# Optimization experiments

Measured on AMD Instinct MI355X. Metric: run time of the kernel, lower is better.

The kernel has to match this reference:

```python
import jax, jax.numpy as jnp
import numpy as np

B, S, D_MODEL, N_HEADS = 4, 2048, 512, 2
D4 = D_MODEL * 4            # output dim of quaternion projections (2048)
HD = D4 // N_HEADS          # per-head dim (1024)
EPS = 1e-6


def quat_linear(x, W, b):
    """Hamilton-product quaternion linear.
    x: [..., 4*in_q] (quaternions interleaved r,i,j,k)
    W: [4, out_q, in_q] components (r,i,j,k); b: [4*out_q]
    returns [..., 4*out_q]
    """
    xq = x.reshape(x.shape[:-1] + (-1, 4))
    xr, xi, xj, xk = xq[..., 0], xq[..., 1], xq[..., 2], xq[..., 3]
    Wr, Wi, Wj, Wk = W[0], W[1], W[2], W[3]
    m = lambda a, M: jnp.einsum('...i,oi->...o', a, M)
    o_r = m(xr, Wr) - m(xi, Wi) - m(xj, Wj) - m(xk, Wk)
    o_i = m(xr, Wi) + m(xi, Wr) + m(xj, Wk) - m(xk, Wj)
    o_j = m(xr, Wj) - m(xi, Wk) + m(xj, Wr) + m(xk, Wi)
    o_k = m(xr, Wk) + m(xi, Wj) - m(xj, Wi) + m(xk, Wr)
    out = jnp.stack([o_r, o_i, o_j, o_k], axis=-1)
    return out.reshape(out.shape[:-2] + (-1,)) + b


def setup_inputs() -> dict:
    rng = jax.random.key(0)
    ks = jax.random.split(rng, 12)
    def w(k, out_q, in_q):
        return jax.random.normal(k, (4, out_q, in_q), jnp.float32) * (1.0 / np.sqrt(4.0 * in_q))
    in_q_small = D_MODEL // 4   # q/k/v projections: d_model reals -> d_model quaternions
    in_q_big = D4 // 4          # later projections: 4*d_model reals -> d_model quaternions
    zb = jnp.zeros((D4,), jnp.float32)
    return {
        'query': jax.random.normal(ks[0], (B, S, D_MODEL), jnp.float32),
        'key':   jax.random.normal(ks[1], (B, S, D_MODEL), jnp.float32),
        'value': jax.random.normal(ks[2], (B, S, D_MODEL), jnp.float32),
        'Wq': w(ks[3], D_MODEL, in_q_small), 'bq': zb,
        'Wk': w(ks[4], D_MODEL, in_q_small), 'bk': zb,
        'Wv': w(ks[5], D_MODEL, in_q_small), 'bv': zb,
        'alpha': jax.random.normal(ks[6], (D4,), jnp.float32) * 0.1,
        'Wint': w(ks[7], D_MODEL, in_q_big), 'bint': zb,
        'Wfin': w(ks[8], D_MODEL, in_q_big), 'bfin': zb,
        'Wout': w(ks[9], D_MODEL, in_q_big), 'bout': zb,
    }


def reference(query, key, value, Wq, bq, Wk, bk, Wv, bv, alpha,
              Wint, bint, Wfin, bfin, Wout, bout):
    Q = quat_linear(query, Wq, bq).reshape(B, S, N_HEADS, HD)
    K = quat_linear(key, Wk, bk).reshape(B, S, N_HEADS, HD)
    V = quat_linear(value, Wv, bv).reshape(B, S, N_HEADS, HD)

    # spectral attention: FFT correlation + adaptive spectral filter
    Qf = jnp.fft.fft(Q, axis=1)
    Kf = jnp.fft.fft(K, axis=1)
    corr = Qf * jnp.conj(Kf)                        # [B,S,H,HD] complex64
    freqs = jnp.abs(jnp.fft.fftfreq(S))             # [S]
    phase = jnp.arctan(jnp.log(freqs + EPS))        # [S]
    a = alpha.reshape(N_HEADS, HD)
    filt = jnp.exp(1j * (phase[:, None, None] * a[None, :, :]))  # [S,H,HD]
    attn_w = jnp.fft.ifft(corr * filt[None], axis=1).real        # [B,S,H,HD]
    attn = (attn_w * V).reshape(B, S, -1)           # [B,S,4*d_model]

    attn = quat_linear(attn, Wint, bint)
    attn = quat_linear(attn, Wfin, bfin)
    return quat_linear(attn, Wout, bout)            # [B,S,4*d_model]
```

## Files before the change

### kernel.cpp

```cpp
#include <hip/hip_runtime.h>
#include <hip/hip_bf16.h>
#include <cstdint>

typedef unsigned short u16;
typedef u16  u16x8 __attribute__((ext_vector_type(8)));
typedef short s16x8 __attribute__((ext_vector_type(8)));
typedef float f32x4 __attribute__((ext_vector_type(4)));

#define PI_F 3.14159265358979323846f
#define PD(i) ((i) + 3 * ((i) >> 5))

static __device__ __forceinline__ u16 f2bf(float f) {
    union { float f; unsigned u; } v; v.f = f;
    unsigned r = v.u + 0x7fffu + ((v.u >> 16) & 1u);
    return (u16)(r >> 16);
}
static __device__ __forceinline__ float bf2f(u16 h) {
    union { unsigned u; float f; } v; v.u = ((unsigned)h) << 16;
    return v.f;
}

__device__ __forceinline__ void gl_lds16(const u16* g, u16* l) {
    __builtin_amdgcn_global_load_lds(
        (const __attribute__((address_space(1))) unsigned int*)g,
        (__attribute__((address_space(3))) unsigned int*)l, 16, 0, 0);
}

__device__ __forceinline__ void cvt_body(int blk, const float* __restrict__ in,
                                         u16* __restrict__ o) {
    int i = blk * 256 + threadIdx.x;
    float4 a = ((const float4*)in)[2 * i];
    float4 b = ((const float4*)in)[2 * i + 1];
    u16x8 vv;
    vv[0] = f2bf(a.x); vv[1] = f2bf(a.y); vv[2] = f2bf(a.z); vv[3] = f2bf(a.w);
    vv[4] = f2bf(b.x); vv[5] = f2bf(b.y); vv[6] = f2bf(b.z); vv[7] = f2bf(b.w);
    ((u16x8*)o)[i] = vv;
}

template<int LOGK>
__device__ __forceinline__ void e3_body(int blk, const float* __restrict__ W,
                                        u16* __restrict__ E) {
    const int K = 1 << LOGK;
    int idx = blk * 256 + threadIdx.x;
    int n = idx >> LOGK, k = idx & (K - 1);
    int o = n >> 2, c = n & 3, i = k >> 2, cp = k & 3;
    const int   qm[4][4] = {{0,1,2,3},{1,0,3,2},{2,3,0,1},{3,2,1,0}};
    const float qs[4][4] = {{1.f,-1.f,-1.f,-1.f},{1.f,1.f,1.f,-1.f},
                            {1.f,-1.f,1.f,1.f},{1.f,1.f,-1.f,1.f}};
    int in_q = K >> 2;
    float w = W[(size_t)qm[c][cp] * 512 * in_q + (size_t)o * in_q + i] * qs[c][cp];
    E[idx] = f2bf(w);
}

__device__ __forceinline__ void tabs_body(int blk, float2* __restrict__ gws,
                                          float* __restrict__ ph) {
    int i = blk * 256 + threadIdx.x;
    if (i < 682) {
        int off, lh;
        if (i < 2)        { off = 0;   lh = 1; }
        else if (i < 10)  { off = 2;   lh = 3; }
        else if (i < 42)  { off = 10;  lh = 5; }
        else if (i < 170) { off = 42;  lh = 7; }
        else              { off = 170; lh = 9; }
        int j = i - off;
        float a = (-PI_F) * (float)j / (float)(2 << lh);
        gws[i] = make_float2(cosf(a), sinf(a));
    }
    if (i <= 1024) {
        ph[i] = atanf(logf((float)i * (1.0f / 2048.0f) + 1e-6f));
    }
}

__global__ __launch_bounds__(256) void fat_prep(
        const float* __restrict__ query, const float* __restrict__ key,
        const float* __restrict__ value, u16* __restrict__ Acvt,
        const float* __restrict__ Wq, const float* __restrict__ Wk,
        const float* __restrict__ Wv, u16* __restrict__ Eq,
        u16* __restrict__ Ek, u16* __restrict__ Ev,
        const float* __restrict__ Wint, const float* __restrict__ Wfin,
        const float* __restrict__ Wout, u16* __restrict__ Eint,
        u16* __restrict__ Efin, u16* __restrict__ Eout,
        float2* __restrict__ gws, float* __restrict__ pht) {
    int b = blockIdx.x;
    if (b < 6144) {
        int ten = b >> 11, r = b & 2047;
        const float* in = (ten == 0) ? query : (ten == 1) ? key : value;
        cvt_body(r, in, Acvt + (size_t)ten * 8192 * 512);
    } else if (b < 18432) {
        int rb = b - 6144;
        int y = rb >> 12, r = rb & 4095;
        e3_body<9>(r, (y == 0) ? Wq : (y == 1) ? Wk : Wv,
                   (y == 0) ? Eq : (y == 1) ? Ek : Ev);
    } else if (b < 67584) {
        int rb = b - 18432;
        int y = rb >> 14, r = rb & 16383;
        e3_body<11>(r, (y == 0) ? Wint : (y == 1) ? Wfin : Wout,
                    (y == 0) ? Eint : (y == 1) ? Efin : Eout);
    } else {
        tabs_body(b - 67584, gws, pht);
    }
}

__global__ __launch_bounds__(256) void matvec_E(const float* __restrict__ v,
                                                const u16* __restrict__ E,
                                                const float* __restrict__ badd,
                                                float* __restrict__ out) {
    int n    = (blockIdx.x * 256 + threadIdx.x) >> 6;
    int lane = threadIdx.x & 63;
    if (n >= 2048) return;
    const u16* row = E + (size_t)n * 2048;
    float s = 0.f;
    for (int j = lane; j < 2048; j += 64) s += v[j] * bf2f(row[j]);
#pragma unroll
    for (int o = 32; o; o >>= 1) s += __shfl_down(s, o, 64);
    if (lane == 0) out[n] = s + badd[n];
}

template<int K, int OUTMODE, int NBY>
__device__ __forceinline__ void gemm_body(int bid, u16* As, u16* Bs,
                                          const u16* __restrict__ A,
                                          const u16* __restrict__ E,
                                          const float* __restrict__ bias,
                                          void* __restrict__ outp) {
    const int t    = threadIdx.x;
    const int lane = t & 63, wave = t >> 6;
    const int wr   = wave >> 1, wc = wave & 1;
    const int lr   = lane & 15, kg = lane >> 4;
    const int l7   = lr & 7;

    constexpr int SPX = (4 * (NBY / 4)) / 8;
    const int xcd = bid & 7, p = bid >> 3;
    const int st  = xcd * SPX + (p >> 4);
    const int w   = p & 15;
    const int bx  = (st & 3) * 4 + (w & 3);
    const int by  = (st >> 2) * 4 + (w >> 2);
    const int m0  = by * 128;
    const int n0  = bx * 128;

    f32x4 acc[4][4];
#pragma unroll
    for (int i = 0; i < 4; ++i)
#pragma unroll
        for (int j = 0; j < 4; ++j) acc[i][j] = (f32x4){0.f, 0.f, 0.f, 0.f};

    const int arow = wr * 64 + lr;
    const int brow = wc * 64 + lr;

    for (int k0 = 0; k0 < K; k0 += 64) {
#pragma unroll
        for (int c = 0; c < 4; ++c) {
            int idx = t + c * 256;
            int row = idx >> 3, sl = idx & 7;
            int gsl = sl ^ (row & 7);
            gl_lds16(A + (size_t)(m0 + row) * K + k0 + gsl * 8, &As[idx * 8]);
            gl_lds16(E + (size_t)(n0 + row) * K + k0 + gsl * 8, &Bs[idx * 8]);
        }
        __syncthreads();
#pragma unroll
        for (int ks = 0; ks < 2; ++ks) {
            const int slot = (ks * 4 + kg) ^ l7;
            s16x8 av[4], bv[4];
#pragma unroll
            for (int mi = 0; mi < 4; ++mi)
                av[mi] = *(const s16x8*)&As[(arow + mi * 16) * 64 + slot * 8];
#pragma unroll
            for (int ni = 0; ni < 4; ++ni)
                bv[ni] = *(const s16x8*)&Bs[(brow + ni * 16) * 64 + slot * 8];
#pragma unroll
            for (int mi = 0; mi < 4; ++mi)
#pragma unroll
                for (int ni = 0; ni < 4; ++ni)
                    acc[mi][ni] = __builtin_amdgcn_mfma_f32_16x16x32_bf16(
                        av[mi], bv[ni], acc[mi][ni], 0, 0, 0);
        }
        __syncthreads();
    }

#pragma unroll
    for (int ni = 0; ni < 4; ++ni) {
        int n = n0 + wc * 64 + ni * 16 + lr;
        float bvl = bias ? bias[n] : 0.0f;
#pragma unroll
        for (int mi = 0; mi < 4; ++mi) {
#pragma unroll
            for (int r = 0; r < 4; ++r) {
                int m = m0 + wr * 64 + mi * 16 + kg * 4 + r;
                float val = acc[mi][ni][r] + bvl;
                if constexpr (OUTMODE == 0) {
                    ((u16*)outp)[(size_t)m * 2048 + n] = f2bf(val);
                } else if constexpr (OUTMODE == 1) {
                    ((float*)outp)[(size_t)m * 2048 + n] = val;
                } else {
                    int b = m >> 11, s = m & 2047;
                    ((u16*)outp)[((size_t)b * 2048 + n) * 2048 + s] = f2bf(val);
                }
            }
        }
    }
}

template<int K, int OUTMODE, int NBY>
__global__ __launch_bounds__(256) void gemm2(const u16* __restrict__ A,
                                             const u16* __restrict__ E,
                                             const float* __restrict__ bias,
                                             void* __restrict__ outp) {
    __shared__ u16 As[128 * 64];
    __shared__ u16 Bs[128 * 64];
    gemm_body<K, OUTMODE, NBY>(blockIdx.x, As, Bs, A, E, bias, outp);
}

__global__ __launch_bounds__(256) void gemm_fat1(const u16* __restrict__ Aq,
                                                 const u16* __restrict__ Eq,
                                                 const float* __restrict__ bq,
                                                 void* __restrict__ Qt,
                                                 const u16* __restrict__ Efin,
                                                 const u16* __restrict__ EintT,
                                                 void* __restrict__ T1T) {
    __shared__ u16 As[128 * 64];
    __shared__ u16 Bs[128 * 64];
    int bid = blockIdx.x;
    if (bid < 256)
        gemm_body<2048, 2, 16>(bid, As, Bs, Efin, EintT, nullptr, T1T);
    else
        gemm_body<512, 2, 64>(bid - 256, As, Bs, Aq, Eq, bq, Qt);
}

__global__ __launch_bounds__(256) void gemm_fat2(const u16* __restrict__ Ak,
                                                 const u16* __restrict__ Ek,
                                                 const float* __restrict__ bk,
                                                 void* __restrict__ Kt,
                                                 const u16* __restrict__ Eout,
                                                 const u16* __restrict__ T1T,
                                                 void* __restrict__ Ecomb) {
    __shared__ u16 As[128 * 64];
    __shared__ u16 Bs[128 * 64];
    int bid = blockIdx.x;
    if (bid < 256)
        gemm_body<2048, 0, 16>(bid, As, Bs, Eout, T1T, nullptr, Ecomb);
    else
        gemm_body<512, 2, 64>(bid - 256, As, Bs, Ak, Ek, bk, Kt);
}

template<int LH, int OFF>
__device__ __forceinline__ void r4pass(float* re, float* im,
                                       const float2* __restrict__ wt, int t) {
    constexpr int h = 1 << LH;
    __syncthreads();
#pragma unroll
    for (int u = 0; u < 2; ++u) {
        int vidx = t + u * 256;
        int j = vidx & (h - 1);
        int i0 = ((vidx >> LH) << (LH + 2)) | j;
        float2 w2 = wt[OFF + j];
        float w1r = w2.x * w2.x - w2.y * w2.y;
        float w1i = 2.f * w2.x * w2.y;
        float w3r = w2.y, w3i = -w2.x;
        int p0 = PD(i0), p1 = PD(i0 + h), p2 = PD(i0 + 2 * h), p3 = PD(i0 + 3 * h);
        float ar = re[p0], ai = im[p0];
        float br = re[p1], bi = im[p1];
        float cr = re[p2], ci = im[p2];
        float dr = re[p3], di = im[p3];
        float tbr = w1r * br - w1i * bi, tbi = w1r * bi + w1i * br;
        float tdr = w1r * dr - w1i * di, tdi = w1r * di + w1i * dr;
        float a1r = ar + tbr, a1i = ai + tbi;
        float b1r = ar - tbr, b1i = ai - tbi;
        float c1r = cr + tdr, c1i = ci + tdi;
        float d1r = cr - tdr, d1i = ci - tdi;
        float tcr = w2.x * c1r - w2.y * c1i, tci = w2.x * c1i + w2.y * c1r;
        float ter = w3r * d1r - w3i * d1i, tei = w3r * d1i + w3i * d1r;
        re[p0] = a1r + tcr; im[p0] = a1i + tci;
        re[p2] = a1r - tcr; im[p2] = a1i - tci;
        re[p1] = b1r + ter; im[p1] = b1i + tei;
        re[p3] = b1r - ter; im[p3] = b1i - tei;
    }
}

__device__ void fft2048(float* re, float* im, const float2* __restrict__ wt, int t) {
    __syncthreads();
#pragma unroll
    for (int u = 0; u < 4; ++u) {
        int i0 = 2 * (t + u * 256);
        int p0 = PD(i0), p1 = p0 + 1;
        float ar = re[p0], ai = im[p0];
        float br = re[p1], bi = im[p1];
        re[p0] = ar + br; im[p0] = ai + bi;
        re[p1] = ar - br; im[p1] = ai - bi;
    }
    r4pass<1, 0>(re, im, wt, t);
    r4pass<3, 2>(re, im, wt, t);
    r4pass<5, 10>(re, im, wt, t);
    r4pass<7, 42>(re, im, wt, t);
    r4pass<9, 170>(re, im, wt, t);
    __syncthreads();
}

__device__ void spectral_body(int sbid, float* zre, float* zim, float2* wt,
                              const u16* __restrict__ Qt,
                              const u16* __restrict__ Kt,
                              u16* __restrict__ Wt,
                              const float* __restrict__ alpha,
                              const float2* __restrict__ gws,
                              const float* __restrict__ gph) {
    const int t  = threadIdx.x;
    const int b  = sbid >> 10;
    const int cp = sbid & 1023;
    const int c0 = cp * 2;
    const size_t base0 = ((size_t)b * 2048 + c0) * 2048;
    const size_t base1 = base0 + 2048;

    for (int i = t; i < 682; i += 256) wt[i] = gws[i];

    float ph[4];
    float PH1r[4], PH1i[4], PH2r[4], PH2i[4];
    float ph24 = 0.f, PH24_1 = 0.f, PH24_2 = 0.f;

#pragma unroll
    for (int ch = 0; ch < 2; ++ch) {
        const size_t base = ch ? base1 : base0;
        const u16* Qp = Qt + base;
        const u16* Kp = Kt + base;
        __syncthreads();
#pragma unroll
        for (int u = 0; u < 8; ++u) {
            int s = t + u * 256;
            int r = __brev((unsigned)s) >> 21;
            zre[PD(r)] = bf2f(Qp[s]);
            zim[PD(r)] = bf2f(Kp[s]);
        }
        fft2048(zre, zim, wt, t);
        const float ac = alpha[c0 + ch];
#pragma unroll
        for (int u = 0; u < 4; ++u) {
            int k = t + u * 256;
            int m = (2048 - k) & 2047;
            float ar = zre[PD(k)], ai = zim[PD(k)];
            float br = zre[PD(m)], bi = zim[PD(m)];
            float qr = 0.5f * (ar + br), qi = 0.5f * (ai - bi);
            float kr = 0.5f * (ai + bi), ki = 0.5f * (br - ar);
            float cr = qr * kr + qi * ki;
            float ci = qi * kr - qr * ki;
            if (ch == 0) ph[u] = gph[min(k, 2048 - k)];
            float fr, fi;
            __sincosf(ph[u] * ac, &fi, &fr);
            float Pkr = cr * fr - ci * fi, Pki = cr * fi + ci * fr;
            float qr2 = 0.5f * (br + ar), qi2 = 0.5f * (bi - ai);
            float kr2 = 0.5f * (bi + ai), ki2 = 0.5f * (ar - br);
            float cr2 = qr2 * kr2 + qi2 * ki2;
            float ci2 = qi2 * kr2 - qr2 * ki2;
            float Pmr = cr2 * fr - ci2 * fi, Pmi = cr2 * fi + ci2 * fr;
            float hr = 0.5f * (Pkr + Pmr), hi = 0.5f * (Pki - Pmi);
            if (ch == 0) { PH1r[u] = hr; PH1i[u] = hi; }
            else         { PH2r[u] = hr; PH2i[u] = hi; }
        }
        if (t == 0) {
            float ar = zre[PD(1024)], ai = zim[PD(1024)];
            float cr = ar * ai;
            if (ch == 0) ph24 = gph[1024];
            float fr, fi;
            __sincosf(ph24 * ac, &fi, &fr);
            if (ch == 0) PH24_1 = cr * fr; else PH24_2 = cr * fr;
        }
    }

    __syncthreads();
#pragma unroll
    for (int u = 0; u < 4; ++u) {
        int k = t + u * 256;
        int m = (2048 - k) & 2047;
        int rk = __brev((unsigned)k) >> 21;
        int rm = __brev((unsigned)m) >> 21;
        zre[PD(rk)] = PH1r[u] - PH2i[u];
        zim[PD(rk)] = PH1i[u] + PH2r[u];
        zre[PD(rm)] = PH1r[u] + PH2i[u];
        zim[PD(rm)] = PH2r[u] - PH1i[u];
    }
    if (t == 0) {
        zre[PD(1)] = PH24_1;
        zim[PD(1)] = PH24_2;
    }
    fft2048(zre, zim, wt, t);

#pragma unroll
    for (int u = 0; u < 8; ++u) {
        int s = t + u * 256;
        int j = (2048 - s) & 2047;
        Wt[base0 + s] = f2bf(zre[PD(j)] * (1.0f / 2048.0f));
        Wt[base1 + s] = f2bf(zim[PD(j)] * (1.0f / 2048.0f));
    }
}

__global__ __launch_bounds__(256) void fat_specv(const u16* __restrict__ Qt,
                                                 const u16* __restrict__ Kt,
                                                 u16* __restrict__ Wt,
                                                 const float* __restrict__ alpha,
                                                 const float2* __restrict__ gws,
                                                 const float* __restrict__ gph,
                                                 const u16* __restrict__ Av,
                                                 const u16* __restrict__ Ev,
                                                 const float* __restrict__ bvb,
                                                 void* __restrict__ Vt) {
    __shared__ __align__(16) char smem[32768];
    int bid = blockIdx.x;
    if (bid % 5 == 4) {
        gemm_body<512, 2, 64>(bid / 5, (u16*)smem, (u16*)(smem + 16384),
                              Av, Ev, bvb, Vt);
    } else {
        int sbid = (bid / 5) * 4 + (bid % 5);
        spectral_body(sbid, (float*)smem, (float*)(smem + 8960),
                      (float2*)(smem + 17920), Qt, Kt, Wt, alpha, gws, gph);
    }
}

__global__ __launch_bounds__(256) void transpose_k(const u16* __restrict__ in,
                                                   u16* __restrict__ out) {
    __shared__ u16 tile[32][33];
    int b = blockIdx.z;
    int c0 = blockIdx.x * 32, s0 = blockIdx.y * 32;
    int tx = threadIdx.x, ty = threadIdx.y;
#pragma unroll
    for (int dy = 0; dy < 32; dy += 8)
        tile[ty + dy][tx] = in[((size_t)b * 2048 + c0 + ty + dy) * 2048 + s0 + tx];
    __syncthreads();
#pragma unroll
    for (int dy = 0; dy < 32; dy += 8)
        out[((size_t)b * 2048 + s0 + ty + dy) * 2048 + c0 + tx] = tile[tx][ty + dy];
}

__global__ __launch_bounds__(256) void transpose_mul(const u16* __restrict__ W,
                                                     const u16* __restrict__ V,
                                                     u16* __restrict__ out) {
    __shared__ u16 tile[32][33];
    int b = blockIdx.z;
    int c0 = blockIdx.x * 32, s0 = blockIdx.y * 32;
    int tx = threadIdx.x, ty = threadIdx.y;
#pragma unroll
    for (int dy = 0; dy < 32; dy += 8) {
        size_t idx = ((size_t)b * 2048 + c0 + ty + dy) * 2048 + s0 + tx;
        tile[ty + dy][tx] = f2bf(bf2f(W[idx]) * bf2f(V[idx]));
    }
    __syncthreads();
#pragma unroll
    for (int dy = 0; dy < 32; dy += 8)
        out[((size_t)b * 2048 + s0 + ty + dy) * 2048 + c0 + tx] = tile[tx][ty + dy];
}

extern "C" void kernel_launch(void* const* d_in, const int* in_sizes, int n_in,
                              void* d_out, int out_size, void* d_ws, size_t ws_size,
                              hipStream_t stream) {
    const float* query = (const float*)d_in[0];
    const float* key   = (const float*)d_in[1];
    const float* value = (const float*)d_in[2];
    const float* Wq    = (const float*)d_in[3];
    const float* bq    = (const float*)d_in[4];
    const float* Wk    = (const float*)d_in[5];
    const float* bk    = (const float*)d_in[6];
    const float* Wv    = (const float*)d_in[7];
    const float* bv    = (const float*)d_in[8];
    const float* alpha = (const float*)d_in[9];
    const float* Wint  = (const float*)d_in[10];
    const float* bint  = (const float*)d_in[11];
    const float* Wfin  = (const float*)d_in[12];
    const float* bfin  = (const float*)d_in[13];
    const float* Wout  = (const float*)d_in[14];
    const float* bout  = (const float*)d_in[15];

    char* ws = (char*)d_ws;
    size_t off = 0;
    auto alloc = [&](size_t bytes) -> void* {
        void* p = ws + off;
        off += (bytes + 255) & ~(size_t)255;
        return p;
    };
    u16* Eq   = (u16*)alloc((size_t)2048 * 512 * 2);
    u16* Ek   = (u16*)alloc((size_t)2048 * 512 * 2);
    u16* Ev   = (u16*)alloc((size_t)2048 * 512 * 2);
    u16* Eint = (u16*)alloc((size_t)2048 * 2048 * 2);
    u16* Efin = (u16*)alloc((size_t)2048 * 2048 * 2);
    u16* Eout = (u16*)alloc((size_t)2048 * 2048 * 2);
    u16* EintT= (u16*)alloc((size_t)2048 * 2048 * 2);
    u16* T1T  = (u16*)alloc((size_t)2048 * 2048 * 2);
    u16* Qt   = (u16*)alloc((size_t)4 * 2048 * 2048 * 2);
    u16* Kt   = (u16*)alloc((size_t)4 * 2048 * 2048 * 2);
    u16* Vt   = (u16*)alloc((size_t)4 * 2048 * 2048 * 2);
    u16* attn = (u16*)alloc((size_t)8192 * 2048 * 2);
    float2* gws = (float2*)alloc(682 * 8);
    float*  pht = (float*)alloc(1025 * 4);
    float*  bv1 = (float*)alloc(2048 * 4);
    float*  bv2 = (float*)alloc(2048 * 4);
    u16* Ecomb = Eint;
    u16* Wt    = Efin;
    u16* Aq = attn;
    u16* Ak = attn + (size_t)8192 * 512;
    u16* Av = attn + (size_t)8192 * 1024;

    fat_prep<<<67589, 256, 0, stream>>>(query, key, value, Aq,
                                        Wq, Wk, Wv, Eq, Ek, Ev,
                                        Wint, Wfin, Wout, Eint, Efin, Eout,
                                        gws, pht);

    dim3 gt1(64, 64, 1);
    transpose_k<<<gt1, dim3(32, 8), 0, stream>>>(Eint, EintT);

    gemm_fat1<<<1280, 256, 0, stream>>>(Aq, Eq, bq, Qt, Efin, EintT, T1T);
    gemm_fat2<<<1280, 256, 0, stream>>>(Ak, Ek, bk, Kt, Eout, T1T, Ecomb);

    matvec_E<<<512, 256, 0, stream>>>(bint, Efin, bfin, bv1);
    matvec_E<<<512, 256, 0, stream>>>(bv1,  Eout, bout, bv2);

    fat_specv<<<5120, 256, 0, stream>>>(Qt, Kt, Wt, alpha, gws, pht,
                                        Av, Ev, bv, Vt);

    dim3 gt(64, 64, 4);
    transpose_mul<<<gt, dim3(32, 8), 0, stream>>>(Wt, Vt, attn);

    gemm2<2048, 1, 64><<<1024, 256, 0, stream>>>(attn, Ecomb, bv2, (float*)d_out);
}
```

Measured before the change: 378.0 us.

## Replace radix-2 plus radix-4 FFT passes with radix-4 first stage and radix-8 passes

```diff
diff --git a/kernel.cpp b/kernel.cpp
--- a/kernel.cpp
+++ b/kernel.cpp
@@ -55,15 +55,12 @@
 __device__ __forceinline__ void tabs_body(int blk, float2* __restrict__ gws,
                                           float* __restrict__ ph) {
     int i = blk * 256 + threadIdx.x;
-    if (i < 682) {
-        int off, lh;
-        if (i < 2)        { off = 0;   lh = 1; }
-        else if (i < 10)  { off = 2;   lh = 3; }
-        else if (i < 42)  { off = 10;  lh = 5; }
-        else if (i < 170) { off = 42;  lh = 7; }
-        else              { off = 170; lh = 9; }
-        int j = i - off;
-        float a = (-PI_F) * (float)j / (float)(2 << lh);
+    if (i < 292) {
+        int off, denom;
+        if (i < 4)       { off = 0;  denom = 16;   }
+        else if (i < 36) { off = 4;  denom = 128;  }
+        else             { off = 36; denom = 1024; }
+        float a = (-PI_F) * (float)(i - off) / (float)denom;
         gws[i] = make_float2(cosf(a), sinf(a));
     }
     if (i <= 1024) {
@@ -242,55 +239,108 @@
 }
 
 template<int LH, int OFF>
-__device__ __forceinline__ void r4pass(float* re, float* im,
+__device__ __forceinline__ void r8pass(float* re, float* im,
                                        const float2* __restrict__ wt, int t) {
     constexpr int h = 1 << LH;
     __syncthreads();
-#pragma unroll
-    for (int u = 0; u < 2; ++u) {
-        int vidx = t + u * 256;
-        int j = vidx & (h - 1);
-        int i0 = ((vidx >> LH) << (LH + 2)) | j;
-        float2 w2 = wt[OFF + j];
-        float w1r = w2.x * w2.x - w2.y * w2.y;
-        float w1i = 2.f * w2.x * w2.y;
-        float w3r = w2.y, w3i = -w2.x;
-        int p0 = PD(i0), p1 = PD(i0 + h), p2 = PD(i0 + 2 * h), p3 = PD(i0 + 3 * h);
-        float ar = re[p0], ai = im[p0];
-        float br = re[p1], bi = im[p1];
-        float cr = re[p2], ci = im[p2];
-        float dr = re[p3], di = im[p3];
-        float tbr = w1r * br - w1i * bi, tbi = w1r * bi + w1i * br;
-        float tdr = w1r * dr - w1i * di, tdi = w1r * di + w1i * dr;
-        float a1r = ar + tbr, a1i = ai + tbi;
-        float b1r = ar - tbr, b1i = ai - tbi;
-        float c1r = cr + tdr, c1i = ci + tdi;
-        float d1r = cr - tdr, d1i = ci - tdi;
-        float tcr = w2.x * c1r - w2.y * c1i, tci = w2.x * c1i + w2.y * c1r;
-        float ter = w3r * d1r - w3i * d1i, tei = w3r * d1i + w3i * d1r;
-        re[p0] = a1r + tcr; im[p0] = a1i + tci;
-        re[p2] = a1r - tcr; im[p2] = a1i - tci;
-        re[p1] = b1r + ter; im[p1] = b1i + tei;
-        re[p3] = b1r - ter; im[p3] = b1i - tei;
-    }
+    const int j  = t & (h - 1);
+    const int i0 = ((t >> LH) << (LH + 3)) | j;
+    const float2 w = wt[OFF + j];
+    const float t2r = w.x * w.x - w.y * w.y;
+    const float t2i = 2.f * w.x * w.y;
+    const float t1r = t2r * t2r - t2i * t2i;
+    const float t1i = 2.f * t2r * t2i;
+    const float S = 0.70710678118654752f;
+    const float Ac = S * (w.x + w.y);
+    const float Bc = S * (w.y - w.x);
+
+    float xr[8], xi[8];
+    int p[8];
+#pragma unroll
+    for (int k = 0; k < 8; ++k) {
+        p[k] = PD(i0 + k * h);
+        xr[k] = re[p[k]]; xi[k] = im[p[k]];
+    }
+#pragma unroll
+    for (int kp = 0; kp < 8; kp += 2) {
+        float tr = t1r * xr[kp + 1] - t1i * xi[kp + 1];
+        float ti = t1r * xi[kp + 1] + t1i * xr[kp + 1];
+        float ar = xr[kp], ai = xi[kp];
+        xr[kp] = ar + tr;     xi[kp] = ai + ti;
+        xr[kp + 1] = ar - tr; xi[kp + 1] = ai - ti;
+    }
+#pragma unroll
+    for (int q = 0; q < 2; ++q) {
+        int b0 = q * 4;
+        {
+            float tr = t2r * xr[b0 + 2] - t2i * xi[b0 + 2];
+            float ti = t2r * xi[b0 + 2] + t2i * xr[b0 + 2];
+            float ar = xr[b0], ai = xi[b0];
+            xr[b0] = ar + tr;     xi[b0] = ai + ti;
+            xr[b0 + 2] = ar - tr; xi[b0 + 2] = ai - ti;
+        }
+        {
+            float tr = t2i * xr[b0 + 3] + t2r * xi[b0 + 3];
+            float ti = t2i * xi[b0 + 3] - t2r * xr[b0 + 3];
+            float ar = xr[b0 + 1], ai = xi[b0 + 1];
+            xr[b0 + 1] = ar + tr; xi[b0 + 1] = ai + ti;
+            xr[b0 + 3] = ar - tr; xi[b0 + 3] = ai - ti;
+        }
+    }
+    {
+        float tr = w.x * xr[4] - w.y * xi[4];
+        float ti = w.x * xi[4] + w.y * xr[4];
+        float ar = xr[0], ai = xi[0];
+        xr[0] = ar + tr; xi[0] = ai + ti;
+        xr[4] = ar - tr; xi[4] = ai - ti;
+    }
+    {
+        float tr = Ac * xr[5] - Bc * xi[5];
+        float ti = Ac * xi[5] + Bc * xr[5];
+        float ar = xr[1], ai = xi[1];
+        xr[1] = ar + tr; xi[1] = ai + ti;
+        xr[5] = ar - tr; xi[5] = ai - ti;
+    }
+    {
+        float tr = w.y * xr[6] + w.x * xi[6];
+        float ti = w.y * xi[6] - w.x * xr[6];
+        float ar = xr[2], ai = xi[2];
+        xr[2] = ar + tr; xi[2] = ai + ti;
+        xr[6] = ar - tr; xi[6] = ai - ti;
+    }
+    {
+        float tr = Bc * xr[7] + Ac * xi[7];
+        float ti = Bc * xi[7] - Ac * xr[7];
+        float ar = xr[3], ai = xi[3];
+        xr[3] = ar + tr; xi[3] = ai + ti;
+        xr[7] = ar - tr; xi[7] = ai - ti;
+    }
+#pragma unroll
+    for (int k = 0; k < 8; ++k) { re[p[k]] = xr[k]; im[p[k]] = xi[k]; }
 }
 
 __device__ void fft2048(float* re, float* im, const float2* __restrict__ wt, int t) {
     __syncthreads();
 #pragma unroll
-    for (int u = 0; u < 4; ++u) {
-        int i0 = 2 * (t + u * 256);
-        int p0 = PD(i0), p1 = p0 + 1;
-        float ar = re[p0], ai = im[p0];
-        float br = re[p1], bi = im[p1];
-        re[p0] = ar + br; im[p0] = ai + bi;
-        re[p1] = ar - br; im[p1] = ai - bi;
-    }
-    r4pass<1, 0>(re, im, wt, t);
-    r4pass<3, 2>(re, im, wt, t);
-    r4pass<5, 10>(re, im, wt, t);
-    r4pass<7, 42>(re, im, wt, t);
-    r4pass<9, 170>(re, im, wt, t);
+    for (int u = 0; u < 2; ++u) {
+        int i0 = (t + u * 256) << 2;
+        int p0 = PD(i0);
+        float x0r = re[p0],     x0i = im[p0];
+        float x1r = re[p0 + 1], x1i = im[p0 + 1];
+        float x2r = re[p0 + 2], x2i = im[p0 + 2];
+        float x3r = re[p0 + 3], x3i = im[p0 + 3];
+        float ar = x0r + x1r, ai = x0i + x1i;
+        float br = x0r - x1r, bi = x0i - x1i;
+        float cr = x2r + x3r, ci = x2i + x3i;
+        float dr = x2r - x3r, di = x2i - x3i;
+        re[p0]     = ar + cr; im[p0]     = ai + ci;
+        re[p0 + 2] = ar - cr; im[p0 + 2] = ai - ci;
+        re[p0 + 1] = br + di; im[p0 + 1] = bi - dr;
+        re[p0 + 3] = br - di; im[p0 + 3] = bi + dr;
+    }
+    r8pass<2, 0>(re, im, wt, t);
+    r8pass<5, 4>(re, im, wt, t);
+    r8pass<8, 36>(re, im, wt, t);
     __syncthreads();
 }
 
@@ -308,7 +358,7 @@
     const size_t base0 = ((size_t)b * 2048 + c0) * 2048;
     const size_t base1 = base0 + 2048;
 
-    for (int i = t; i < 682; i += 256) wt[i] = gws[i];
+    for (int i = t; i < 292; i += 256) wt[i] = gws[i];
 
     float ph[4];
     float PH1r[4], PH1i[4], PH2r[4], PH2i[4];
@@ -483,7 +533,7 @@
     u16* Kt   = (u16*)alloc((size_t)4 * 2048 * 2048 * 2);
     u16* Vt   = (u16*)alloc((size_t)4 * 2048 * 2048 * 2);
     u16* attn = (u16*)alloc((size_t)8192 * 2048 * 2);
-    float2* gws = (float2*)alloc(682 * 8);
+    float2* gws = (float2*)alloc(292 * 8);
     float*  pht = (float*)alloc(1025 * 4);
     float*  bv1 = (float*)alloc(2048 * 4);
     float*  bv2 = (float*)alloc(2048 * 4);
```

Result: no change. 373.4 us (-1.2%).
